# Optimization experiments

Measured on AMD Instinct MI355X. Metric: run time of the kernel, lower is better.

## Reference

```python
import jax, jax.numpy as jnp
import numpy as np
import math

NUM_BUCKETS = 32
MAX_DISTANCE = 128


def _relative_position_bucket(relative_position):
    # Unidirectional (bidirectional=False): rp = max(-relative_position, 0)
    rp = jnp.maximum(-relative_position, 0)
    max_exact = NUM_BUCKETS // 2  # 16
    is_small = rp < max_exact
    rp_f = jnp.maximum(rp, 1).astype(jnp.float32)
    large = max_exact + (
        jnp.log(rp_f / max_exact) / math.log(MAX_DISTANCE / max_exact)
        * (NUM_BUCKETS - max_exact)
    ).astype(jnp.int32)
    large = jnp.minimum(large, NUM_BUCKETS - 1)
    return jnp.where(is_small, rp, large)


def _t5_rel_bias(bias_table, T):
    # bias_table: [num_buckets, n_heads] -> [1, n_heads, T, T]
    ctx = jnp.arange(T, dtype=jnp.int32)[:, None]
    mem = jnp.arange(T, dtype=jnp.int32)[None, :]
    buckets = _relative_position_bucket(mem - ctx)  # [T, T]
    values = bias_table[buckets]  # [T, T, H]
    return jnp.transpose(values, (2, 0, 1))[None]  # [1, H, T, T]


def setup_inputs() -> dict:
    key = jax.random.key(0)
    ks = jax.random.split(key, 6)
    B, T, C, H = 2, 2048, 1024, 16
    x = jax.random.normal(ks[0], (B, T, C), dtype=jnp.float32)
    W_attn = jax.random.normal(ks[1], (C, 3 * C), dtype=jnp.float32) * 0.02
    b_attn = jnp.zeros((3 * C,), dtype=jnp.float32)
    W_proj = jax.random.normal(ks[2], (C, C), dtype=jnp.float32) * 0.02
    b_proj = jnp.zeros((C,), dtype=jnp.float32)
    bias_table = jax.random.normal(ks[3], (NUM_BUCKETS, H), dtype=jnp.float32) * 0.02
    return {"x": x, "W_attn": W_attn, "b_attn": b_attn,
            "W_proj": W_proj, "b_proj": b_proj, "bias_table": bias_table}


def reference(x, W_attn, b_attn, W_proj, b_proj, bias_table):
    B, T, C = x.shape
    H = bias_table.shape[1]
    D = C // H
    qkv = x @ W_attn + b_attn  # [B, T, 3C]
    q, k, v = jnp.split(qkv, 3, axis=-1)
    # [B, T, C] -> [B, H, T, D]
    q = q.reshape(B, T, H, D).transpose(0, 2, 1, 3)
    k = k.reshape(B, T, H, D).transpose(0, 2, 1, 3)
    v = v.reshape(B, T, H, D).transpose(0, 2, 1, 3)
    rel_bias = _t5_rel_bias(bias_table, T)  # [1, H, T, T]
    att = jnp.einsum('bhtd,bhsd->bhts', q, k) * (1.0 / math.sqrt(D))
    att = att + rel_bias
    causal = jnp.tril(jnp.ones((T, T), dtype=bool))
    att = jnp.where(causal, att, -jnp.inf)
    att = jax.nn.softmax(att, axis=-1)
    y = jnp.einsum('bhts,bhsd->bhtd', att, v)  # [B, H, T, D]
    y = y.transpose(0, 2, 1, 3).reshape(B, T, C)
    return y @ W_proj + b_proj
```

## Files before the change

kernel.cpp:

```cpp
#include <hip/hip_runtime.h>
#include <hip/hip_bf16.h>
#include <math.h>

typedef __attribute__((ext_vector_type(4))) float f32x4;
typedef __attribute__((ext_vector_type(8))) __bf16 bf16x8;
typedef __attribute__((ext_vector_type(4))) __bf16 bf16x4;

#define DEVI __device__ __forceinline__

DEVI f32x4 mfma16(bf16x8 a, bf16x8 b, f32x4 c) {
  return __builtin_amdgcn_mfma_f32_16x16x32_bf16(a, b, c, 0, 0, 0);
}

DEVI void gload16(const void* g, void* l) {
  __builtin_amdgcn_global_load_lds(
      (const __attribute__((address_space(1))) void*)g,
      (__attribute__((address_space(3))) void*)l, 16, 0, 0);
}

DEVI float exp2a(float x) {
  float r;
  asm("v_exp_f32 %0, %1" : "=v"(r) : "v"(x));
  return r;
}

#define LOG2E 1.4426950408889634f
#define QSCALE 0.18033688011110793f

__global__ __launch_bounds__(256) void prep_k(
    const float* __restrict__ x, const float* __restrict__ W_attn,
    const float* __restrict__ W_proj, const float* __restrict__ bt,
    __bf16* __restrict__ xb, __bf16* __restrict__ WaT,
    __bf16* __restrict__ WpT, float* __restrict__ tbl) {
  __shared__ float tile[32][33];
  int bid = blockIdx.x;
  const int t = threadIdx.x;
  if (bid < 4096) {
    int i = (bid * 256 + t) * 4;
    float4 v = *(const float4*)&x[i];
    bf16x4 o = {(__bf16)v.x, (__bf16)v.y, (__bf16)v.z, (__bf16)v.w};
    *(bf16x4*)&xb[i] = o;
    return;
  }
  bid -= 4096;
  if (bid < 4096) {
    const float* in;
    __bf16* out;
    int Cc, bx, by;
    if (bid < 3072) {
      in = W_attn; out = WaT; Cc = 3072; bx = bid % 96; by = bid / 96;
    } else {
      int b2 = bid - 3072;
      in = W_proj; out = WpT; Cc = 1024; bx = b2 % 32; by = b2 / 32;
    }
    const int R = 1024;
    int tx = t & 31, ty = t >> 5;
    int xcol = bx * 32 + tx;
    for (int r = ty; r < 32; r += 8)
      tile[r][tx] = in[(size_t)(by * 32 + r) * Cc + xcol];
    __syncthreads();
    int xo = by * 32 + tx;
    for (int r = ty; r < 32; r += 8)
      out[(size_t)(bx * 32 + r) * R + xo] = (__bf16)tile[tx][r];
    return;
  }
  bid -= 4096;
  int idx = bid * 256 + t;
  int h = idx >> 11, rp = idx & 2047;
  int bucket;
  if (rp < 16) {
    bucket = rp;
  } else {
    float v = (logf((float)rp * 0.0625f) / 2.0794415416798357f) * 16.0f;
    bucket = 16 + (int)v;
    if (bucket > 31) bucket = 31;
  }
  tbl[idx] = bt[bucket * 16 + h] * LOG2E;
}

template <int MODE>
__global__ __launch_bounds__(256) void gemm_bf16(
    const __bf16* __restrict__ A, const __bf16* __restrict__ BT,
    const float* __restrict__ bias, float* __restrict__ outF,
    __bf16* __restrict__ qb, __bf16* __restrict__ kb, __bf16* __restrict__ vtb,
    int M, int N, int K) {
  __shared__ __align__(16) __bf16 lA[128 * 32];
  __shared__ __align__(16) __bf16 lB[128 * 32];
  const int t = threadIdx.x;
  const int w = t >> 6, lane = t & 63;
  const int m0 = blockIdx.x * 128, n0 = blockIdx.y * 128;
  const int wr = (w >> 1) * 64, wc = (w & 1) * 64;

  f32x4 acc[4][4] = {};

  const int rA = lane & 15;
  const int kk = (lane >> 4) * 8;

  for (int k0 = 0; k0 < K; k0 += 32) {
    __syncthreads();
#pragma unroll
    for (int r = 0; r < 2; ++r) {
      int c = r * 256 + t;
      int row = c >> 2, cc = c & 3;
      gload16(A + (size_t)(m0 + row) * K + k0 + cc * 8,
              &lA[(r * 256 + w * 64) * 8]);
      gload16(BT + (size_t)(n0 + row) * K + k0 + cc * 8,
              &lB[(r * 256 + w * 64) * 8]);
    }
    __syncthreads();
    bf16x8 af[4], bfr[4];
#pragma unroll
    for (int i = 0; i < 4; ++i)
      af[i] = *(const bf16x8*)&lA[(wr + i * 16 + rA) * 32 + kk];
#pragma unroll
    for (int j = 0; j < 4; ++j)
      bfr[j] = *(const bf16x8*)&lB[(wc + j * 16 + rA) * 32 + kk];
#pragma unroll
    for (int i = 0; i < 4; ++i)
#pragma unroll
      for (int j = 0; j < 4; ++j)
        acc[i][j] = mfma16(af[i], bfr[j], acc[i][j]);
  }

  const int colb = n0 + wc + rA;
  const int rowb = m0 + wr + (lane >> 4) * 4;
#pragma unroll
  for (int j = 0; j < 4; ++j) {
    int n = colb + j * 16;
    float bv = bias[n];
#pragma unroll
    for (int i = 0; i < 4; ++i) {
#pragma unroll
      for (int e = 0; e < 4; ++e) {
        int m = rowb + i * 16 + e;
        float v = acc[i][j][e] + bv;
        if constexpr (MODE == 0) {
          int b = m >> 11, tt = m & 2047;
          int sec = n >> 10, nn = n & 1023;
          int h = nn >> 6, d = nn & 63;
          if (sec == 0)
            qb[(((size_t)(b * 16 + h)) * 2048 + tt) * 64 + d] = (__bf16)(v * QSCALE);
          else if (sec == 1)
            kb[(((size_t)(b * 16 + h)) * 2048 + tt) * 64 + d] = (__bf16)v;
          else
            vtb[(((size_t)(b * 16 + h)) * 64 + d) * 2048 + tt] = (__bf16)v;
        } else {
          outF[(size_t)m * N + n] = v;
        }
      }
    }
  }
}

__global__ __launch_bounds__(256) void attn_k(
    const __bf16* __restrict__ q, const __bf16* __restrict__ k,
    const __bf16* __restrict__ vt, const float* __restrict__ tbl,
    __bf16* __restrict__ y) {
  __shared__ __align__(16) __bf16 lK[2][64 * 64];
  __shared__ __align__(16) __bf16 lV[2][64 * 64];
  __shared__ __align__(16) __bf16 lPT[4][16 * 64];
  __shared__ float lb[2][128];

  const int t = threadIdx.x, w = t >> 6, lane = t & 63;
  const int bh = blockIdx.x, b = bh >> 4, h = bh & 15;
  const int qt = (gridDim.y - 1) - blockIdx.y;
  const int qbase = qt * 64 + w * 16;
  const int kq = lane >> 4, ncol = lane & 15;
  const int sw = (ncol & 7);

  const __bf16* qp = q + (size_t)bh * 2048 * 64;
  const __bf16* kp = k + (size_t)bh * 2048 * 64;
  const __bf16* vp = vt + (size_t)bh * 64 * 2048;
  const float* tb = tbl + h * 2048;
  const float bconst = tb[2047];

  bf16x8 qf0 = *(const bf16x8*)&qp[(size_t)(qbase + ncol) * 64 + kq * 8];
  bf16x8 qf1 = *(const bf16x8*)&qp[(size_t)(qbase + ncol) * 64 + kq * 8 + 32];

  f32x4 O[4] = {};
  float m = -INFINITY, lsum = 0.f;
  __bf16* Pw = &lPT[w][0];

  auto STAGE = [&](int buf, int jt) {
    int dt = qt - jt;
#pragma unroll
    for (int r = 0; r < 2; ++r) {
      int c = r * 256 + t;
      int row = c >> 3, cc = c & 7;
      int sc = cc ^ (row & 7);
      gload16(kp + (size_t)(jt * 64 + row) * 64 + sc * 8,
              &lK[buf][(r * 256 + w * 64) * 8]);
      gload16(vp + (size_t)row * 2048 + jt * 64 + sc * 8,
              &lV[buf][(r * 256 + w * 64) * 8]);
    }
    if (dt < 3 && t < 128) {
      int rb = dt * 64 - 63 + t;
      lb[buf][t] = tb[rb < 0 ? 0 : rb];
    }
  };

  STAGE(0, 0);
  int cur = 0;
  for (int jt = 0; jt <= qt; ++jt, cur ^= 1) {
    const int dt = qt - jt;
    const bool diag = (jt == qt);
    __syncthreads();
    if (jt < qt) STAGE(cur ^ 1, jt + 1);

    const __bf16* Kc = lK[cur];
    const float* lbc = lb[cur];

    float pv[4][4];
    const int idxb = 63 + w * 16 + ncol - 4 * kq;
    float tm = -INFINITY;
#pragma unroll
    for (int fn = 0; fn < 4; ++fn) {
      if (!diag || fn <= w) {
        f32x4 s;
        if (dt >= 3) {
          s = (f32x4){bconst, bconst, bconst, bconst};
        } else {
#pragma unroll
          for (int i = 0; i < 4; ++i) s[i] = lbc[idxb - fn * 16 - i];
          if (diag && fn == w) {
#pragma unroll
            for (int i = 0; i < 4; ++i)
              if (ncol - 4 * kq - i < 0) s[i] = -1e30f;
          }
        }
        int row = fn * 16 + ncol;
        bf16x8 kf0 = *(const bf16x8*)((const char*)Kc + row * 128 + ((kq ^ sw) * 16));
        bf16x8 kf1 = *(const bf16x8*)((const char*)Kc + row * 128 + (((4 + kq) ^ sw) * 16));
        s = mfma16(kf0, qf0, s);
        s = mfma16(kf1, qf1, s);
#pragma unroll
        for (int i = 0; i < 4; ++i) {
          pv[fn][i] = s[i];
          tm = fmaxf(tm, s[i]);
        }
      }
    }
    tm = fmaxf(tm, __shfl_xor(tm, 16));
    tm = fmaxf(tm, __shfl_xor(tm, 32));

    if (__any(tm > m + 8.f)) {
      float mn = fmaxf(m, tm);
      float corr = exp2a(m - mn);
      m = mn;
      lsum *= corr;
#pragma unroll
      for (int i = 0; i < 4; ++i) {
        float ci = __shfl(corr, 4 * kq + i);
#pragma unroll
        for (int fd = 0; fd < 4; ++fd) O[fd][i] *= ci;
      }
    }

#pragma unroll
    for (int fn = 0; fn < 4; ++fn) {
      bf16x4 pb;
      if (!diag || fn <= w) {
#pragma unroll
        for (int i = 0; i < 4; ++i) {
          float p = exp2a(pv[fn][i] - m);
          lsum += p;
          pb[i] = (__bf16)p;
        }
      } else {
        pb = (bf16x4){(__bf16)0.f, (__bf16)0.f, (__bf16)0.f, (__bf16)0.f};
      }
      *(bf16x4*)((char*)Pw + ncol * 128 + ((32 * fn + 8 * kq) ^ (sw << 4))) = pb;
    }
    asm volatile("s_waitcnt lgkmcnt(0)" ::: "memory");
    __builtin_amdgcn_sched_barrier(0);

    const __bf16* Vc = lV[cur];
    const int kf2max = (diag && w < 2) ? 1 : 2;
    for (int kf2 = 0; kf2 < kf2max; ++kf2) {
      bf16x8 pf = *(const bf16x8*)((const char*)Pw + ncol * 128 +
                                   (((4 * kf2 + kq) ^ sw) * 16));
#pragma unroll
      for (int fd = 0; fd < 4; ++fd) {
        int vrow = fd * 16 + ncol;
        bf16x8 vf = *(const bf16x8*)((const char*)Vc + vrow * 128 +
                                     (((4 * kf2 + kq) ^ sw) * 16));
        O[fd] = mfma16(pf, vf, O[fd]);
      }
    }
  }

  lsum += __shfl_xor(lsum, 16);
  lsum += __shfl_xor(lsum, 32);
#pragma unroll
  for (int i = 0; i < 4; ++i) {
    float li = __shfl(lsum, 4 * kq + i);
    float rinv = 1.0f / li;
    int row = qbase + 4 * kq + i;
#pragma unroll
    for (int fd = 0; fd < 4; ++fd) {
      int col = h * 64 + fd * 16 + ncol;
      y[((size_t)(b * 2048 + row)) * 1024 + col] = (__bf16)(O[fd][i] * rinv);
    }
  }
}


extern "C" void kernel_launch(void* const* d_in, const int* in_sizes, int n_in,
                              void* d_out, int out_size, void* d_ws, size_t ws_size,
                              hipStream_t stream) {
  const float* x = (const float*)d_in[0];
  const float* W_attn = (const float*)d_in[1];
  const float* b_attn = (const float*)d_in[2];
  const float* W_proj = (const float*)d_in[3];
  const float* b_proj = (const float*)d_in[4];
  const float* bias_table = (const float*)d_in[5];
  float* out = (float*)d_out;

  char* ws = (char*)d_ws;
  __bf16* xb   = (__bf16*)(ws + 0);
  __bf16* WaT  = (__bf16*)(ws + 8388608);
  __bf16* WpT  = (__bf16*)(ws + 14680064);
  __bf16* qb   = (__bf16*)(ws + 16777216);
  __bf16* kb   = (__bf16*)(ws + 25165824);
  __bf16* vtb  = (__bf16*)(ws + 33554432);
  __bf16* yb   = (__bf16*)(ws + 41943040);
  float*  tbl  = (float*)(ws + 50331648);

  prep_k<<<8320, 256, 0, stream>>>(x, W_attn, W_proj, bias_table,
                                   xb, WaT, WpT, tbl);
  gemm_bf16<0><<<dim3(32, 24), 256, 0, stream>>>(xb, WaT, b_attn, nullptr,
                                                 qb, kb, vtb, 4096, 3072, 1024);
  attn_k<<<dim3(32, 32), 256, 0, stream>>>(qb, kb, vtb, tbl, yb);
  gemm_bf16<1><<<dim3(32, 8), 256, 0, stream>>>(yb, WpT, b_proj, out,
                                                nullptr, nullptr, nullptr,
                                                4096, 1024, 1024);
}
```

Measured before the change: 130.3 us.

## Process 128 query rows per attention block with 8 waves sharing K/V tiles

The attention kernel now runs 512 threads (8 waves) per block covering 128 query rows instead of 64, so each staged 64-row K/V tile in LDS is reused by twice as many waves. The grid halves along the query axis, each thread issues a single K and V load per stage, and per-wave causal masking is recomputed from a relative tile offset. Waves whose rows lie entirely before a key tile skip compute but still take part in the barriers. This halves K/V global traffic and staging overhead per query, at the cost of fewer blocks for load balancing and idle waves on the diagonal tiles.

```diff
diff --git a/kernel.cpp b/kernel.cpp
--- a/kernel.cpp
+++ b/kernel.cpp
@@ -152,19 +152,19 @@
   }
 }
 
-__global__ __launch_bounds__(256) void attn_k(
+__global__ __launch_bounds__(512) void attn_k(
     const __bf16* __restrict__ q, const __bf16* __restrict__ k,
     const __bf16* __restrict__ vt, const float* __restrict__ tbl,
     __bf16* __restrict__ y) {
   __shared__ __align__(16) __bf16 lK[2][64 * 64];
   __shared__ __align__(16) __bf16 lV[2][64 * 64];
-  __shared__ __align__(16) __bf16 lPT[4][16 * 64];
-  __shared__ float lb[2][128];
+  __shared__ __align__(16) __bf16 lPT[8][16 * 64];
+  __shared__ float lb[2][192];
 
   const int t = threadIdx.x, w = t >> 6, lane = t & 63;
   const int bh = blockIdx.x, b = bh >> 4, h = bh & 15;
-  const int qt = (gridDim.y - 1) - blockIdx.y;
-  const int qbase = qt * 64 + w * 16;
+  const int qt2 = (gridDim.y - 1) - blockIdx.y;
+  const int qbase = qt2 * 128 + w * 16;
   const int kq = lane >> 4, ncol = lane & 15;
   const int sw = (ncol & 7);
 
@@ -181,48 +181,46 @@
   float m = -INFINITY, lsum = 0.f;
   __bf16* Pw = &lPT[w][0];
 
+  const int srow = t >> 3, scc = t & 7;
+  const int ssc = scc ^ (srow & 7);
+
   auto STAGE = [&](int buf, int jt) {
-    int dt = qt - jt;
-#pragma unroll
-    for (int r = 0; r < 2; ++r) {
-      int c = r * 256 + t;
-      int row = c >> 3, cc = c & 7;
-      int sc = cc ^ (row & 7);
-      gload16(kp + (size_t)(jt * 64 + row) * 64 + sc * 8,
-              &lK[buf][(r * 256 + w * 64) * 8]);
-      gload16(vp + (size_t)row * 2048 + jt * 64 + sc * 8,
-              &lV[buf][(r * 256 + w * 64) * 8]);
-    }
-    if (dt < 3 && t < 128) {
-      int rb = dt * 64 - 63 + t;
+    gload16(kp + (size_t)(jt * 64 + srow) * 64 + ssc * 8, &lK[buf][w * 512]);
+    gload16(vp + (size_t)srow * 2048 + jt * 64 + ssc * 8, &lV[buf][w * 512]);
+    int dtb = 2 * qt2 - jt;
+    if (dtb < 3 && t < 192) {
+      int rb = dtb * 64 - 63 + t;
       lb[buf][t] = tb[rb < 0 ? 0 : rb];
     }
   };
 
+  const int jtmax = 2 * qt2 + 1;
   STAGE(0, 0);
   int cur = 0;
-  for (int jt = 0; jt <= qt; ++jt, cur ^= 1) {
-    const int dt = qt - jt;
-    const bool diag = (jt == qt);
+  for (int jt = 0; jt <= jtmax; ++jt, cur ^= 1) {
+    const int dtb = 2 * qt2 - jt;
+    const int rel = 4 * dtb + w;
     __syncthreads();
-    if (jt < qt) STAGE(cur ^ 1, jt + 1);
+    if (jt < jtmax) STAGE(cur ^ 1, jt + 1);
+    if (rel < 0) continue;
 
     const __bf16* Kc = lK[cur];
     const float* lbc = lb[cur];
+    const bool useb = (dtb >= 3);
 
     float pv[4][4];
     const int idxb = 63 + w * 16 + ncol - 4 * kq;
     float tm = -INFINITY;
 #pragma unroll
     for (int fn = 0; fn < 4; ++fn) {
-      if (!diag || fn <= w) {
+      if (fn <= rel) {
         f32x4 s;
-        if (dt >= 3) {
+        if (useb) {
           s = (f32x4){bconst, bconst, bconst, bconst};
         } else {
 #pragma unroll
           for (int i = 0; i < 4; ++i) s[i] = lbc[idxb - fn * 16 - i];
-          if (diag && fn == w) {
+          if (fn == rel) {
 #pragma unroll
             for (int i = 0; i < 4; ++i)
               if (ncol - 4 * kq - i < 0) s[i] = -1e30f;
@@ -259,7 +257,7 @@
 #pragma unroll
     for (int fn = 0; fn < 4; ++fn) {
       bf16x4 pb;
-      if (!diag || fn <= w) {
+      if (fn <= rel) {
 #pragma unroll
         for (int i = 0; i < 4; ++i) {
           float p = exp2a(pv[fn][i] - m);
@@ -275,7 +273,7 @@
     __builtin_amdgcn_sched_barrier(0);
 
     const __bf16* Vc = lV[cur];
-    const int kf2max = (diag && w < 2) ? 1 : 2;
+    const int kf2max = (rel >= 2) ? 2 : 1;
     for (int kf2 = 0; kf2 < kf2max; ++kf2) {
       bf16x8 pf = *(const bf16x8*)((const char*)Pw + ncol * 128 +
                                    (((4 * kf2 + kq) ^ sw) * 16));
@@ -330,7 +328,7 @@
                                    xb, WaT, WpT, tbl);
   gemm_bf16<0><<<dim3(32, 24), 256, 0, stream>>>(xb, WaT, b_attn, nullptr,
                                                  qb, kb, vtb, 4096, 3072, 1024);
-  attn_k<<<dim3(32, 32), 256, 0, stream>>>(qb, kb, vtb, tbl, yb);
+  attn_k<<<dim3(32, 16), 512, 0, stream>>>(qb, kb, vtb, tbl, yb);
   gemm_bf16<1><<<dim3(32, 8), 256, 0, stream>>>(yb, WpT, b_proj, out,
                                                 nullptr, nullptr, nullptr,
                                                 4096, 1024, 1024);
```

Result: no change. 132.7 us (+1.9%).
